# Kernel tuning notes

Measured on AMD Instinct MI355X. Metric: run time of the kernel, lower is better.

The kernel has to match this reference:

```python
import jax, jax.numpy as jnp
import numpy as np

B, N, D_IN, D_OUT = 4, 2048, 1024, 1024

def setup_inputs() -> dict:
    key = jax.random.key(0)
    ks = jax.random.split(key, 7)
    s_in = 1.0 / np.sqrt(D_IN)
    return {
        "X": jax.random.normal(ks[0], (B, N, D_IN), dtype=jnp.float32),
        "Wq": jax.random.uniform(ks[1], (D_IN, D_OUT), jnp.float32, -s_in, s_in),
        "bq": jax.random.uniform(ks[2], (D_OUT,), jnp.float32, -s_in, s_in),
        "Wk": jax.random.uniform(ks[3], (D_IN, D_OUT), jnp.float32, -s_in, s_in),
        "bk": jax.random.uniform(ks[4], (D_OUT,), jnp.float32, -s_in, s_in),
        "Wv": jax.random.uniform(ks[5], (D_IN, D_OUT), jnp.float32, -s_in, s_in),
        "bv": jax.random.uniform(ks[6], (D_OUT,), jnp.float32, -s_in, s_in),
    }

def reference(X, Wq, bq, Wk, bk, Wv, bv):
    # QKV projections: [B,N,D_in] @ [D_in,D_out] -> [B,N,D_out]
    q = jnp.einsum('bnd,de->bne', X, Wq) + bq
    k = jnp.einsum('bnd,de->bne', X, Wk) + bk
    v = jnp.einsum('bnd,de->bne', X, Wv) + bv
    # Unscaled attention (faithful: original has no 1/sqrt(d))
    scores = jnp.einsum('bne,bme->bnm', q, k)  # [B,N,N]
    weights = jax.nn.softmax(scores, axis=-1)
    return jnp.einsum('bnm,bme->bne', weights, v)
```

## Files before the change

### kernel.cpp

```cpp
#include <hip/hip_runtime.h>
#include <hip/hip_bf16.h>
#include <hip/hip_fp16.h>
#include <stdint.h>
#include <math.h>


typedef unsigned short ushort_t;
typedef __attribute__((ext_vector_type(8))) _Float16  f16x8;
typedef __attribute__((ext_vector_type(4))) _Float16  f16x4;
typedef __attribute__((ext_vector_type(4))) float     f32x4;

__device__ __forceinline__ void async_load16(const void* g, void* l) {
  __builtin_amdgcn_global_load_lds(
      (const __attribute__((address_space(1))) void*)g,
      (__attribute__((address_space(3))) void*)l, 16, 0, 0);
}

#define BARR do { __builtin_amdgcn_sched_barrier(0); \
                  __builtin_amdgcn_s_barrier();      \
                  __builtin_amdgcn_sched_barrier(0); } while (0)

#define A0OFF 0
#define B0OFF 16384
#define A1OFF 32768
#define B1OFF 49152

template<int SHIFT>
__device__ __forceinline__ void stage_half(const ushort_t* __restrict__ gb,
                                           int k0, int q, ushort_t* lt, int t)
{
#pragma unroll
  for (int j = 0; j < 2; ++j) {
    const int i   = j * 64 + (t >> 3);
    const int row = ((i >> SHIFT) << (SHIFT + 1)) | (q << SHIFT) | (i & ((1 << SHIFT) - 1));
    const int ch  = (t & 7) ^ (row & 7);
    async_load16(gb + (long)row * 1024 + k0 + ch * 8, lt + row * 64 + (t & 7) * 8);
  }
}

#define RD_A(TP, QM)                                                          \
  do { _Pragma("unroll") for (int m_ = 0; m_ < 4; ++m_) {                     \
    af[m_][0] = *(const f16x8*)&(TP)[(arow0 + (QM)*64 + m_*16) * 64 + ck0];   \
    af[m_][1] = *(const f16x8*)&(TP)[(arow0 + (QM)*64 + m_*16) * 64 + ck1];   \
  } } while (0)

#define RD_B(TP, QN)                                                          \
  do { _Pragma("unroll") for (int n_ = 0; n_ < 2; ++n_) {                     \
    bf[n_][0] = *(const f16x8*)&(TP)[(brow0 + (QN)*32 + n_*16) * 64 + ck0];   \
    bf[n_][1] = *(const f16x8*)&(TP)[(brow0 + (QN)*32 + n_*16) * 64 + ck1];   \
  } } while (0)

#define MM(QM, QN)                                                            \
  do { __builtin_amdgcn_s_setprio(1);                                         \
  _Pragma("unroll") for (int kh_ = 0; kh_ < 2; ++kh_)                         \
    _Pragma("unroll") for (int m_ = 0; m_ < 4; ++m_)                          \
      _Pragma("unroll") for (int n_ = 0; n_ < 2; ++n_)                        \
        acc[(QM)*4+m_][(QN)*2+n_] = __builtin_amdgcn_mfma_f32_16x16x32_f16(   \
            af[m_][kh_], bf[n_][kh_], acc[(QM)*4+m_][(QN)*2+n_], 0, 0, 0);    \
  __builtin_amdgcn_s_setprio(0); } while (0)

template<bool LAST>
__device__ __forceinline__ void iter256(const ushort_t* __restrict__ Ab,
                                        const ushort_t* __restrict__ Bb,
                                        ushort_t* lds, f32x4 (&acc)[8][4],
                                        int ka, int t, int arow0, int brow0,
                                        int ck0, int ck1)
{
  const int kb = ka + 64, kc = ka + 128, kd = ka + 192;
  f16x8 af[4][2], bf[2][2];

  RD_A(lds + A0OFF, 0); RD_B(lds + B0OFF, 0);
  stage_half<5>(Bb, kb, 0, lds + B1OFF, t);
  BARR; MM(0, 0); BARR;

  RD_B(lds + B0OFF, 1);
  if constexpr (!LAST) stage_half<6>(Ab, kc, 0, lds + A0OFF, t);
  BARR; MM(0, 1); BARR;

  RD_A(lds + A0OFF, 1);
  if constexpr (!LAST) stage_half<5>(Bb, kc, 1, lds + B0OFF, t);
  BARR; MM(1, 1); BARR;

  RD_B(lds + B0OFF, 0);
  if constexpr (!LAST) stage_half<6>(Ab, kc, 1, lds + A0OFF, t);
  BARR; MM(1, 0);
  if constexpr (LAST) asm volatile("s_waitcnt vmcnt(0)" ::: "memory");
  else                asm volatile("s_waitcnt vmcnt(6)" ::: "memory");
  BARR;

  RD_A(lds + A1OFF, 0); RD_B(lds + B1OFF, 0);
  if constexpr (!LAST) stage_half<5>(Bb, kc, 0, lds + B0OFF, t);
  BARR; MM(0, 0); BARR;

  RD_B(lds + B1OFF, 1);
  if constexpr (!LAST) stage_half<6>(Ab, kd, 0, lds + A1OFF, t);
  BARR; MM(0, 1); BARR;

  RD_A(lds + A1OFF, 1);
  if constexpr (!LAST) stage_half<5>(Bb, kd, 1, lds + B1OFF, t);
  BARR; MM(1, 1); BARR;

  RD_B(lds + B1OFF, 0);
  if constexpr (!LAST) stage_half<6>(Ab, kd, 1, lds + A1OFF, t);
  BARR; MM(1, 0);
  if constexpr (!LAST) asm volatile("s_waitcnt vmcnt(6)" ::: "memory");
  BARR;
}

__device__ __forceinline__ void gemm256(const ushort_t* __restrict__ Ab,
                                        const ushort_t* __restrict__ Bb,
                                        ushort_t* lds, f32x4 (&acc)[8][4])
{
  const int t    = threadIdx.x;
  const int lane = t & 63;
  const int wave = t >> 6;
  const int wr   = wave >> 2;
  const int wc   = wave & 3;
  const int arow0 = wr * 128 + (lane & 15);
  const int brow0 = wc * 64  + (lane & 15);
  const int ck0 = (((lane >> 4)    ) ^ (lane & 7)) * 8;
  const int ck1 = ((4 + (lane >> 4)) ^ (lane & 7)) * 8;

  stage_half<6>(Ab,  0, 0, lds + A0OFF, t);
  stage_half<5>(Bb,  0, 1, lds + B0OFF, t);
  stage_half<6>(Ab,  0, 1, lds + A0OFF, t);
  stage_half<5>(Bb,  0, 0, lds + B0OFF, t);
  stage_half<6>(Ab, 64, 0, lds + A1OFF, t);
  stage_half<5>(Bb, 64, 1, lds + B1OFF, t);
  stage_half<6>(Ab, 64, 1, lds + A1OFF, t);
  asm volatile("s_waitcnt vmcnt(6)" ::: "memory");
  BARR;

#pragma unroll 1
  for (int it = 0; it < 7; ++it)
    iter256<false>(Ab, Bb, lds, acc, it * 128, t, arow0, brow0, ck0, ck1);
  iter256<true>(Ab, Bb, lds, acc, 896, t, arow0, brow0, ck0, ck1);
}

#define NA0 0
#define NB0 16384
#define NA1 24576
#define NB1 40960

__device__ __forceinline__ void stage_A_n(const ushort_t* __restrict__ gb, long ldk,
                                          int k0, int q, ushort_t* lt, int t)
{
#pragma unroll
  for (int j = 0; j < 2; ++j) {
    const int i   = j * 64 + (t >> 3);
    const int row = ((i >> 5) << 6) | (q << 5) | (i & 31);
    const int ch  = (t & 7) ^ (row & 7);
    async_load16(gb + (long)row * ldk + k0 + ch * 8, lt + row * 64 + (t & 7) * 8);
  }
}

__device__ __forceinline__ void stage_B_n(const ushort_t* __restrict__ gb, long ldk,
                                          int k0, int q, ushort_t* lt, int t)
{
  const int i   = t >> 3;
  const int row = ((i >> 5) << 6) | (q << 5) | (i & 31);
  const int ch  = (t & 7) ^ (row & 7);
  async_load16(gb + (long)row * ldk + k0 + ch * 8, lt + row * 64 + (t & 7) * 8);
}

#define RDN_A(TP, QM)                                                         \
  do { _Pragma("unroll") for (int m_ = 0; m_ < 2; ++m_) {                     \
    af[m_][0] = *(const f16x8*)&(TP)[(arow_l + (QM)*32 + m_*16) * 64 + ck0];  \
    af[m_][1] = *(const f16x8*)&(TP)[(arow_l + (QM)*32 + m_*16) * 64 + ck1];  \
  } } while (0)

#define RDN_AS(TP, QM, S)                                                     \
  do { _Pragma("unroll") for (int m_ = 0; m_ < 2; ++m_) {                     \
    af[m_][0] = *(const f16x8*)&(TP)[(arow_l + (QM)*32 + m_*16) * 64 + ck0] * (S)[(QM)*2+m_]; \
    af[m_][1] = *(const f16x8*)&(TP)[(arow_l + (QM)*32 + m_*16) * 64 + ck1] * (S)[(QM)*2+m_]; \
  } } while (0)

#define RDN_B(TP, QN)                                                         \
  do { _Pragma("unroll") for (int n_ = 0; n_ < 2; ++n_) {                     \
    bf[n_][0] = *(const f16x8*)&(TP)[(brow_l + (QN)*32 + n_*16) * 64 + ck0];  \
    bf[n_][1] = *(const f16x8*)&(TP)[(brow_l + (QN)*32 + n_*16) * 64 + ck1];  \
  } } while (0)

#define MMN(QM, QN)                                                           \
  do { __builtin_amdgcn_s_setprio(1);                                         \
  _Pragma("unroll") for (int kh_ = 0; kh_ < 2; ++kh_)                         \
    _Pragma("unroll") for (int m_ = 0; m_ < 2; ++m_)                          \
      _Pragma("unroll") for (int n_ = 0; n_ < 2; ++n_)                        \
        acc[(QM)*2+m_][(QN)*2+n_] = __builtin_amdgcn_mfma_f32_16x16x32_f16(   \
            af[m_][kh_], bf[n_][kh_], acc[(QM)*2+m_][(QN)*2+n_], 0, 0, 0);    \
  __builtin_amdgcn_s_setprio(0); } while (0)

template<bool LAST>
__device__ __forceinline__ void iter_n(const ushort_t* __restrict__ Ab,
                                       const ushort_t* __restrict__ Bb,
                                       long lda, long ldb,
                                       ushort_t* lds, f32x4 (&acc)[4][4],
                                       int ka, int t, int arow_l, int brow_l,
                                       int ck0, int ck1)
{
  const int kb = ka + 64, kc = ka + 128, kd = ka + 192;
  f16x8 af[2][2], bf[2][2];

  RDN_A(lds + NA0, 0); RDN_B(lds + NB0, 0);
  stage_B_n(Bb, ldb, kb, 0, lds + NB1, t);
  BARR; MMN(0, 0); BARR;

  RDN_B(lds + NB0, 1);
  if constexpr (!LAST) stage_A_n(Ab, lda, kc, 0, lds + NA0, t);
  BARR; MMN(0, 1); BARR;

  RDN_A(lds + NA0, 1);
  if constexpr (!LAST) stage_B_n(Bb, ldb, kc, 1, lds + NB0, t);
  BARR; MMN(1, 1); BARR;

  RDN_B(lds + NB0, 0);
  if constexpr (!LAST) stage_A_n(Ab, lda, kc, 1, lds + NA0, t);
  BARR; MMN(1, 0);
  if constexpr (LAST) asm volatile("s_waitcnt vmcnt(0)" ::: "memory");
  else                asm volatile("s_waitcnt vmcnt(5)" ::: "memory");
  BARR;

  RDN_A(lds + NA1, 0); RDN_B(lds + NB1, 0);
  if constexpr (!LAST) stage_B_n(Bb, ldb, kc, 0, lds + NB0, t);
  BARR; MMN(0, 0); BARR;

  RDN_B(lds + NB1, 1);
  if constexpr (!LAST) stage_A_n(Ab, lda, kd, 0, lds + NA1, t);
  BARR; MMN(0, 1); BARR;

  RDN_A(lds + NA1, 1);
  if constexpr (!LAST) stage_B_n(Bb, ldb, kd, 1, lds + NB1, t);
  BARR; MMN(1, 1); BARR;

  RDN_B(lds + NB1, 0);
  if constexpr (!LAST) stage_A_n(Ab, lda, kd, 1, lds + NA1, t);
  BARR; MMN(1, 0);
  if constexpr (!LAST) asm volatile("s_waitcnt vmcnt(5)" ::: "memory");
  BARR;
}

template<bool LAST>
__device__ __forceinline__ void pv_iter_n(const ushort_t* __restrict__ Ab,
                                          const ushort_t* __restrict__ Bb,
                                          ushort_t* lds, f32x4 (&acc)[4][4],
                                          int ka, int t, int arow_l, int brow_l,
                                          int ck0, int ck1,
                                          float (&scc)[2][4],
                                          const float* __restrict__ Scb, int arow_abs)
{
  const int kb = ka + 64, kc = ka + 128, kd = ka + 192;
  f16x8 af[2][2], bf[2][2];

  float scn[2][4];
  if constexpr (!LAST) {
    const int cbn = (ka >> 6) + 2;
#pragma unroll
    for (int h = 0; h < 2; ++h)
#pragma unroll
      for (int s = 0; s < 4; ++s)
        scn[h][s] = Scb[(long)(cbn + h) * 2048 + arow_abs + s * 16];
  }
  _Float16 sa[4], sb[4];
#pragma unroll
  for (int s = 0; s < 4; ++s) { sa[s] = (_Float16)scc[0][s]; sb[s] = (_Float16)scc[1][s]; }

  RDN_AS(lds + NA0, 0, sa); RDN_B(lds + NB0, 0);
  stage_B_n(Bb, 2048, kb, 0, lds + NB1, t);
  BARR; MMN(0, 0); BARR;

  RDN_B(lds + NB0, 1);
  if constexpr (!LAST) stage_A_n(Ab, 2048, kc, 0, lds + NA0, t);
  BARR; MMN(0, 1); BARR;

  RDN_AS(lds + NA0, 1, sa);
  if constexpr (!LAST) stage_B_n(Bb, 2048, kc, 1, lds + NB0, t);
  BARR; MMN(1, 1); BARR;

  RDN_B(lds + NB0, 0);
  if constexpr (!LAST) stage_A_n(Ab, 2048, kc, 1, lds + NA0, t);
  BARR; MMN(1, 0);
  if constexpr (LAST) asm volatile("s_waitcnt vmcnt(0)" ::: "memory");
  else                asm volatile("s_waitcnt vmcnt(5)" ::: "memory");
  BARR;

  RDN_AS(lds + NA1, 0, sb); RDN_B(lds + NB1, 0);
  if constexpr (!LAST) stage_B_n(Bb, 2048, kc, 0, lds + NB0, t);
  BARR; MMN(0, 0); BARR;

  RDN_B(lds + NB1, 1);
  if constexpr (!LAST) stage_A_n(Ab, 2048, kd, 0, lds + NA1, t);
  BARR; MMN(0, 1); BARR;

  RDN_AS(lds + NA1, 1, sb);
  if constexpr (!LAST) stage_B_n(Bb, 2048, kd, 1, lds + NB1, t);
  BARR; MMN(1, 1); BARR;

  RDN_B(lds + NB1, 0);
  if constexpr (!LAST) stage_A_n(Ab, 2048, kd, 1, lds + NA1, t);
  BARR; MMN(1, 0);
  if constexpr (!LAST) asm volatile("s_waitcnt vmcnt(5)" ::: "memory");
  BARR;

  if constexpr (!LAST) {
#pragma unroll
    for (int h = 0; h < 2; ++h)
#pragma unroll
      for (int s = 0; s < 4; ++s) scc[h][s] = scn[h][s];
  }
}

#define PROLOGUE_N(LDA, LDB)                                \
  do {                                                      \
    stage_A_n(Ab, (LDA),  0, 0, lds + NA0, t);              \
    stage_B_n(Bb, (LDB),  0, 0, lds + NB0, t);              \
    stage_A_n(Ab, (LDA),  0, 1, lds + NA0, t);              \
    stage_B_n(Bb, (LDB),  0, 1, lds + NB0, t);              \
    stage_A_n(Ab, (LDA), 64, 0, lds + NA1, t);              \
    stage_B_n(Bb, (LDB), 64, 1, lds + NB1, t);              \
    stage_A_n(Ab, (LDA), 64, 1, lds + NA1, t);              \
    asm volatile("s_waitcnt vmcnt(5)" ::: "memory");        \
    BARR;                                                   \
  } while (0)

__global__ __launch_bounds__(512, 2)
void qkv128n_kernel(const ushort_t* __restrict__ A, const ushort_t* __restrict__ BT,
                    const float* __restrict__ bq, const float* __restrict__ bk,
                    const float* __restrict__ bvp,
                    __half* __restrict__ Qh, __half* __restrict__ Kh,
                    ushort_t* __restrict__ Vt)
{
  __shared__ __align__(16) ushort_t lds[49152];

  const int nb = gridDim.x * gridDim.y;
  int id = blockIdx.y * gridDim.x + blockIdx.x;
  id = (id & 7) * (nb >> 3) + (id >> 3);
  const int bx = id % gridDim.x;
  const int by = id / gridDim.x;

  const ushort_t* Ab = A  + (long)by * 256 * 1024;
  const ushort_t* Bb = BT + (long)bx * 128 * 1024;

  const int t    = threadIdx.x;
  const int lane = t & 63;
  const int wave = t >> 6;
  const int wr   = wave >> 1;
  const int wc   = wave & 1;
  const int arow_l = wr * 64 + (lane & 15);
  const int brow_l = wc * 64 + (lane & 15);
  const int ck0 = (((lane >> 4)    ) ^ (lane & 7)) * 8;
  const int ck1 = ((4 + (lane >> 4)) ^ (lane & 7)) * 8;

  f32x4 acc[4][4];
  const f32x4 zero = {0.0f, 0.0f, 0.0f, 0.0f};
#pragma unroll
  for (int i = 0; i < 4; ++i)
#pragma unroll
    for (int j = 0; j < 4; ++j) acc[i][j] = zero;

  PROLOGUE_N(1024, 1024);
#pragma unroll 1
  for (int it = 0; it < 7; ++it)
    iter_n<false>(Ab, Bb, 1024, 1024, lds, acc, it * 128, t, arow_l, brow_l, ck0, ck1);
  iter_n<true>(Ab, Bb, 1024, 1024, lds, acc, 896, t, arow_l, brow_l, ck0, ck1);

  const int er = (lane >> 4) * 4, ec = lane & 15;
  const int tgt = bx >> 3;
  const float* bias = (tgt == 0) ? bq : (tgt == 1) ? bk : bvp;

#pragma unroll
  for (int ni = 0; ni < 4; ++ni) {
    const int col = (bx & 7) * 128 + wc * 64 + ni * 16 + ec;
    const float bval = bias[col];
#pragma unroll
    for (int mi = 0; mi < 4; ++mi) {
      const long grow0 = (long)by * 256 + wr * 64 + mi * 16 + er;
      if (tgt < 2) {
        __half* o = (tgt == 0) ? Qh : Kh;
#pragma unroll
        for (int r = 0; r < 4; ++r)
          o[(grow0 + r) * 1024 + col] = __float2half(acc[mi][ni][r] + bval);
      } else {
        const long b  = grow0 >> 11;
        const long ml = grow0 & 2047;
        f16x4 v4;
#pragma unroll
        for (int r = 0; r < 4; ++r) v4[r] = (_Float16)(acc[mi][ni][r] + bval);
        *(f16x4*)&Vt[b * 2097152 + (long)col * 2048 + ml] = v4;
      }
    }
  }
}

__global__ __launch_bounds__(512, 2)
void qk256_kernel(const ushort_t* __restrict__ Q, const ushort_t* __restrict__ Kh,
                  __half* __restrict__ S, float* __restrict__ PM, float* __restrict__ PS)
{
  __shared__ __align__(16) ushort_t lds[65536];

  const int nb = gridDim.x * gridDim.y;
  int id = blockIdx.y * gridDim.x + blockIdx.x;
  id = (id & 7) * (nb >> 3) + (id >> 3);
  const int bx = id % gridDim.x;
  const int by = id / gridDim.x;
  const long z = blockIdx.z;

  const ushort_t* Ab = Q  + z * 2048 * 1024 + (long)by * 256 * 1024;
  const ushort_t* Bb = Kh + z * 2048 * 1024 + (long)bx * 256 * 1024;
  __half* Sb = S + z * 2048 * 2048;

  f32x4 acc[8][4];
  const f32x4 zero = {0.0f, 0.0f, 0.0f, 0.0f};
#pragma unroll
  for (int i = 0; i < 8; ++i)
#pragma unroll
    for (int j = 0; j < 4; ++j) acc[i][j] = zero;

  gemm256(Ab, Bb, lds, acc);

  const int t = threadIdx.x, lane = t & 63, wave = t >> 6;
  const int wr = wave >> 2, wc = wave & 3;
  const int er = (lane >> 4) * 4, ec = lane & 15;
  const int cc = bx * 4 + wc;
  float* PMb = PM + z * 32 * 2048 + (long)cc * 2048;
  float* PSb = PS + z * 32 * 2048 + (long)cc * 2048;

#pragma unroll
  for (int m8 = 0; m8 < 8; ++m8)
#pragma unroll
    for (int r = 0; r < 4; ++r) {
      float m = fmaxf(fmaxf(acc[m8][0][r], acc[m8][1][r]),
                      fmaxf(acc[m8][2][r], acc[m8][3][r]));
      m = fmaxf(m, __shfl_xor(m, 1));
      m = fmaxf(m, __shfl_xor(m, 2));
      m = fmaxf(m, __shfl_xor(m, 4));
      m = fmaxf(m, __shfl_xor(m, 8));
      float s = 0.0f;
#pragma unroll
      for (int n4 = 0; n4 < 4; ++n4) {
        const float e = __expf(acc[m8][n4][r] - m);
        acc[m8][n4][r] = e;
        s += e;
      }
      s += __shfl_xor(s, 1);
      s += __shfl_xor(s, 2);
      s += __shfl_xor(s, 4);
      s += __shfl_xor(s, 8);
      if (ec == 0) {
        const long row = (long)by * 256 + wr * 128 + m8 * 16 + er + r;
        PMb[row] = m;
        PSb[row] = s;
      }
    }

#pragma unroll
  for (int n4 = 0; n4 < 4; ++n4) {
    const long col = (long)bx * 256 + wc * 64 + n4 * 16 + ec;
#pragma unroll
    for (int m8 = 0; m8 < 8; ++m8)
#pragma unroll
      for (int r = 0; r < 4; ++r) {
        const long grow = (long)by * 256 + wr * 128 + m8 * 16 + er + r;
        Sb[grow * 2048 + col] = __float2half(acc[m8][n4][r]);
      }
  }
}

__global__ __launch_bounds__(256)
void softmax_reduce_kernel(const float* __restrict__ PM, const float* __restrict__ PS,
                           float* __restrict__ Sc)
{
  const int r = blockIdx.x * 256 + threadIdx.x;
  const int b = r >> 11, row = r & 2047;
  const long base = (long)b * 32 * 2048 + row;
  float m = -3.4e38f;
#pragma unroll
  for (int cb = 0; cb < 32; ++cb) m = fmaxf(m, PM[base + cb * 2048]);
  float l = 0.0f;
#pragma unroll
  for (int cb = 0; cb < 32; ++cb) l += PS[base + cb * 2048] * __expf(PM[base + cb * 2048] - m);
  const float inv = 1.0f / l;
#pragma unroll
  for (int cb = 0; cb < 32; ++cb) Sc[base + cb * 2048] = __expf(PM[base + cb * 2048] - m) * inv;
}

__global__ __launch_bounds__(512, 2)
void pv128n_kernel(const ushort_t* __restrict__ S, const ushort_t* __restrict__ Vt,
                   const float* __restrict__ Sc, float* __restrict__ Out)
{
  __shared__ __align__(16) ushort_t lds[49152];

  const int nb = gridDim.x * gridDim.y;
  int id = blockIdx.y * gridDim.x + blockIdx.x;
  id = (id & 7) * (nb >> 3) + (id >> 3);
  const int bx = id % gridDim.x;
  const int by = id / gridDim.x;
  const long z = blockIdx.z;

  const ushort_t* Ab = S  + z * 4194304 + (long)by * 256 * 2048;
  const ushort_t* Bb = Vt + z * 2097152 + (long)bx * 128 * 2048;
  const float* Scb = Sc + z * 32 * 2048;
  float* Cb = Out + z * 2048 * 1024;

  const int t    = threadIdx.x;
  const int lane = t & 63;
  const int wave = t >> 6;
  const int wr   = wave >> 1;
  const int wc   = wave & 1;
  const int arow_l = wr * 64 + (lane & 15);
  const int brow_l = wc * 64 + (lane & 15);
  const int arow_abs = by * 256 + arow_l;
  const int ck0 = (((lane >> 4)    ) ^ (lane & 7)) * 8;
  const int ck1 = ((4 + (lane >> 4)) ^ (lane & 7)) * 8;

  f32x4 acc[4][4];
  const f32x4 zero = {0.0f, 0.0f, 0.0f, 0.0f};
#pragma unroll
  for (int i = 0; i < 4; ++i)
#pragma unroll
    for (int j = 0; j < 4; ++j) acc[i][j] = zero;

  float scc[2][4];
#pragma unroll
  for (int h = 0; h < 2; ++h)
#pragma unroll
    for (int s = 0; s < 4; ++s)
      scc[h][s] = Scb[(long)h * 2048 + arow_abs + s * 16];

  PROLOGUE_N(2048, 2048);
#pragma unroll 1
  for (int it = 0; it < 15; ++it)
    pv_iter_n<false>(Ab, Bb, lds, acc, it * 128, t, arow_l, brow_l, ck0, ck1,
                     scc, Scb, arow_abs);
  pv_iter_n<true>(Ab, Bb, lds, acc, 1920, t, arow_l, brow_l, ck0, ck1,
                  scc, Scb, arow_abs);

  const int er = (lane >> 4) * 4, ec = lane & 15;
#pragma unroll
  for (int ni = 0; ni < 4; ++ni) {
    const int gcol = bx * 128 + wc * 64 + ni * 16 + ec;
#pragma unroll
    for (int mi = 0; mi < 4; ++mi) {
#pragma unroll
      for (int r = 0; r < 4; ++r) {
        const long grow = (long)by * 256 + wr * 64 + mi * 16 + er + r;
        Cb[grow * 1024 + gcol] = acc[mi][ni][r];
      }
    }
  }
}

__global__ __launch_bounds__(256)
void cvt_f32_f16_kernel(const float* __restrict__ src, __half* __restrict__ dst, long n)
{
  const long i = ((long)blockIdx.x * 256 + threadIdx.x) * 8;
  if (i + 8 > n) return;
  const float4 a = *(const float4*)(src + i);
  const float4 b = *(const float4*)(src + i + 4);
  f16x8 h;
  h[0] = (_Float16)a.x; h[1] = (_Float16)a.y; h[2] = (_Float16)a.z; h[3] = (_Float16)a.w;
  h[4] = (_Float16)b.x; h[5] = (_Float16)b.y; h[6] = (_Float16)b.z; h[7] = (_Float16)b.w;
  *(f16x8*)((ushort_t*)dst + i) = h;
}

__global__ __launch_bounds__(256)
void transpose_cvt3_kernel(const float* __restrict__ W0, const float* __restrict__ W1,
                           const float* __restrict__ W2, __half* __restrict__ dst)
{
  __shared__ float tile[32][33];
  const int z = blockIdx.z;
  const float* src = (z == 0) ? W0 : (z == 1) ? W1 : W2;
  __half* d = dst + (long)z * 1024 * 1024;
  const int c0 = blockIdx.x * 32;
  const int r0 = blockIdx.y * 32;
  const int tx = threadIdx.x & 31;
  const int ty = threadIdx.x >> 5;
#pragma unroll
  for (int i = 0; i < 32; i += 8)
    tile[ty + i][tx] = src[(long)(r0 + ty + i) * 1024 + (c0 + tx)];
  __syncthreads();
#pragma unroll
  for (int i = 0; i < 32; i += 8)
    d[(long)(c0 + ty + i) * 1024 + (r0 + tx)] = __float2half(tile[tx][ty + i]);
}

extern "C" void kernel_launch(void* const* d_in, const int* in_sizes, int n_in,
                              void* d_out, int out_size, void* d_ws, size_t ws_size,
                              hipStream_t stream)
{
  const int  Bb = 4, Nn = 2048, Dd = 1024;
  const long BN = (long)Bb * Nn;

  const float* X  = (const float*)d_in[0];
  const float* Wq = (const float*)d_in[1];
  const float* bq = (const float*)d_in[2];
  const float* Wk = (const float*)d_in[3];
  const float* bk = (const float*)d_in[4];
  const float* Wv = (const float*)d_in[5];
  const float* bv = (const float*)d_in[6];
  float* Out      = (float*)d_out;

  uint8_t* w = (uint8_t*)d_ws;
  ushort_t* Wt = (ushort_t*)w;  w += (size_t)3 * Dd * Dd * 2;

  transpose_cvt3_kernel<<<dim3(Dd / 32, Dd / 32, 3), 256, 0, stream>>>(Wq, Wk, Wv, (__half*)Wt);

  const size_t statsBytes = (size_t)Bb * 32 * Nn * 4;
  const size_t fullNeed = (size_t)3 * Dd * Dd * 2
                        + 4 * ((size_t)BN * Dd * 2)
                        + (size_t)Bb * Nn * Nn * 2
                        + 3 * statsBytes;

  if (ws_size >= fullNeed) {
    ushort_t* Xh = (ushort_t*)w;  w += (size_t)BN * Dd * 2;
    ushort_t* Q  = (ushort_t*)w;  w += (size_t)BN * Dd * 2;
    ushort_t* Kb = (ushort_t*)w;  w += (size_t)BN * Dd * 2;
    ushort_t* Vt = (ushort_t*)w;  w += (size_t)BN * Dd * 2;
    ushort_t* S  = (ushort_t*)w;  w += (size_t)Bb * Nn * Nn * 2;
    float*    PM = (float*)w;     w += statsBytes;
    float*    PS = (float*)w;     w += statsBytes;
    float*    Sc = (float*)w;

    cvt_f32_f16_kernel<<<dim3((unsigned)(BN * Dd / (8 * 256))), 256, 0, stream>>>(
        X, (__half*)Xh, BN * Dd);

    qkv128n_kernel<<<dim3(3 * Dd / 128, BN / 256, 1), 512, 0, stream>>>(
        Xh, Wt, bq, bk, bv, (__half*)Q, (__half*)Kb, Vt);

    qk256_kernel<<<dim3(Nn / 256, Nn / 256, Bb), 512, 0, stream>>>(
        Q, Kb, (__half*)S, PM, PS);

    softmax_reduce_kernel<<<dim3((unsigned)(Bb * Nn / 256)), 256, 0, stream>>>(PM, PS, Sc);

    pv128n_kernel<<<dim3(Dd / 128, Nn / 256, Bb), 512, 0, stream>>>(
        S, Vt, Sc, Out);
  } else {
    ushort_t* Xh = (ushort_t*)w;  w += (size_t)Nn * Dd * 2;
    ushort_t* Q  = (ushort_t*)w;  w += (size_t)Nn * Dd * 2;
    ushort_t* Kb = (ushort_t*)w;  w += (size_t)Nn * Dd * 2;
    ushort_t* Vt = (ushort_t*)w;  w += (size_t)Nn * Dd * 2;
    ushort_t* S  = (ushort_t*)w;  w += (size_t)Nn * Nn * 2;
    float*    PM = (float*)w;     w += (size_t)32 * Nn * 4;
    float*    PS = (float*)w;     w += (size_t)32 * Nn * 4;
    float*    Sc = (float*)w;

    for (int b = 0; b < Bb; ++b) {
      const float* Xb = X + (long)b * Nn * Dd;
      cvt_f32_f16_kernel<<<dim3((unsigned)((long)Nn * Dd / (8 * 256))), 256, 0, stream>>>(
          Xb, (__half*)Xh, (long)Nn * Dd);
      qkv128n_kernel<<<dim3(3 * Dd / 128, Nn / 256, 1), 512, 0, stream>>>(
          Xh, Wt, bq, bk, bv, (__half*)Q, (__half*)Kb, Vt);
      qk256_kernel<<<dim3(Nn / 256, Nn / 256, 1), 512, 0, stream>>>(
          Q, Kb, (__half*)S, PM, PS);
      softmax_reduce_kernel<<<dim3((unsigned)(Nn / 256)), 256, 0, stream>>>(PM, PS, Sc);
      pv128n_kernel<<<dim3(Dd / 128, Nn / 256, 1), 512, 0, stream>>>(
          S, Vt, Sc, Out + (long)b * Nn * Dd);
    }
  }
}
```

Measured before the change: 267.3 us.

## Fuse softmax reduce into PV, merge prep kernels, restructure GEMM inner pipeline

The softmax row-statistics reduction is folded into the PV kernel: each block computes per-chunk scale factors into shared memory rather than reading a separate Sc buffer. The weight transpose and X conversion are merged into one prep launch. The GEMM inner loop now reads both B column-halves at once and runs 4 MFMA phases per 128-K step instead of 8, which halves the barriers and changes the staging order and vmcnt thresholds. This removes two launches and a global round trip for the scales. In exchange each PV block recomputes the row reduction, adds 32KB of shared memory, and holds more registers.

```diff
diff --git a/kernel.cpp b/kernel.cpp
--- a/kernel.cpp
+++ b/kernel.cpp
@@ -175,159 +175,143 @@
     af[m_][1] = *(const f16x8*)&(TP)[(arow_l + (QM)*32 + m_*16) * 64 + ck1] * (S)[(QM)*2+m_]; \
   } } while (0)
 
-#define RDN_B(TP, QN)                                                         \
+#define RDN_B2(TP, QN, BF)                                                    \
   do { _Pragma("unroll") for (int n_ = 0; n_ < 2; ++n_) {                     \
-    bf[n_][0] = *(const f16x8*)&(TP)[(brow_l + (QN)*32 + n_*16) * 64 + ck0];  \
-    bf[n_][1] = *(const f16x8*)&(TP)[(brow_l + (QN)*32 + n_*16) * 64 + ck1];  \
+    (BF)[n_][0] = *(const f16x8*)&(TP)[(brow_l + (QN)*32 + n_*16) * 64 + ck0];\
+    (BF)[n_][1] = *(const f16x8*)&(TP)[(brow_l + (QN)*32 + n_*16) * 64 + ck1];\
   } } while (0)
 
-#define MMN(QM, QN)                                                           \
+#define MM2(QM)                                                               \
   do { __builtin_amdgcn_s_setprio(1);                                         \
   _Pragma("unroll") for (int kh_ = 0; kh_ < 2; ++kh_)                         \
     _Pragma("unroll") for (int m_ = 0; m_ < 2; ++m_)                          \
-      _Pragma("unroll") for (int n_ = 0; n_ < 2; ++n_)                        \
-        acc[(QM)*2+m_][(QN)*2+n_] = __builtin_amdgcn_mfma_f32_16x16x32_f16(   \
-            af[m_][kh_], bf[n_][kh_], acc[(QM)*2+m_][(QN)*2+n_], 0, 0, 0);    \
+      _Pragma("unroll") for (int n_ = 0; n_ < 2; ++n_) {                      \
+        acc[(QM)*2+m_][n_]   = __builtin_amdgcn_mfma_f32_16x16x32_f16(        \
+            af[m_][kh_], bq0[n_][kh_], acc[(QM)*2+m_][n_], 0, 0, 0);          \
+        acc[(QM)*2+m_][2+n_] = __builtin_amdgcn_mfma_f32_16x16x32_f16(        \
+            af[m_][kh_], bq1[n_][kh_], acc[(QM)*2+m_][2+n_], 0, 0, 0);        \
+      }                                                                       \
   __builtin_amdgcn_s_setprio(0); } while (0)
 
 template<bool LAST>
-__device__ __forceinline__ void iter_n(const ushort_t* __restrict__ Ab,
-                                       const ushort_t* __restrict__ Bb,
-                                       long lda, long ldb,
-                                       ushort_t* lds, f32x4 (&acc)[4][4],
-                                       int ka, int t, int arow_l, int brow_l,
-                                       int ck0, int ck1)
+__device__ __forceinline__ void iter4_n(const ushort_t* __restrict__ Ab,
+                                        const ushort_t* __restrict__ Bb,
+                                        long lda, long ldb,
+                                        ushort_t* lds, f32x4 (&acc)[4][4],
+                                        int ka, int t, int arow_l, int brow_l,
+                                        int ck0, int ck1)
 {
   const int kb = ka + 64, kc = ka + 128, kd = ka + 192;
-  f16x8 af[2][2], bf[2][2];
-
-  RDN_A(lds + NA0, 0); RDN_B(lds + NB0, 0);
-  stage_B_n(Bb, ldb, kb, 0, lds + NB1, t);
-  BARR; MMN(0, 0); BARR;
-
-  RDN_B(lds + NB0, 1);
-  if constexpr (!LAST) stage_A_n(Ab, lda, kc, 0, lds + NA0, t);
-  BARR; MMN(0, 1); BARR;
+  f16x8 af[2][2], bq0[2][2], bq1[2][2];
+
+  RDN_A(lds + NA0, 0);
+  RDN_B2(lds + NB0, 0, bq0);
+  RDN_B2(lds + NB0, 1, bq1);
+  stage_B_n(Bb, ldb, kb, 1, lds + NB1, t);
+  stage_A_n(Ab, lda, kb, 1, lds + NA1, t);
+  BARR; MM2(0); BARR;
 
   RDN_A(lds + NA0, 1);
-  if constexpr (!LAST) stage_B_n(Bb, ldb, kc, 1, lds + NB0, t);
-  BARR; MMN(1, 1); BARR;
-
-  RDN_B(lds + NB0, 0);
-  if constexpr (!LAST) stage_A_n(Ab, lda, kc, 1, lds + NA0, t);
-  BARR; MMN(1, 0);
+  if constexpr (!LAST) {
+    stage_A_n(Ab, lda, kc, 0, lds + NA0, t);
+    stage_B_n(Bb, ldb, kc, 0, lds + NB0, t);
+  }
+  BARR; MM2(1);
   if constexpr (LAST) asm volatile("s_waitcnt vmcnt(0)" ::: "memory");
-  else                asm volatile("s_waitcnt vmcnt(5)" ::: "memory");
+  else                asm volatile("s_waitcnt vmcnt(3)" ::: "memory");
   BARR;
 
-  RDN_A(lds + NA1, 0); RDN_B(lds + NB1, 0);
-  if constexpr (!LAST) stage_B_n(Bb, ldb, kc, 0, lds + NB0, t);
-  BARR; MMN(0, 0); BARR;
-
-  RDN_B(lds + NB1, 1);
-  if constexpr (!LAST) stage_A_n(Ab, lda, kd, 0, lds + NA1, t);
-  BARR; MMN(0, 1); BARR;
+  RDN_A(lds + NA1, 0);
+  RDN_B2(lds + NB1, 0, bq0);
+  RDN_B2(lds + NB1, 1, bq1);
+  if constexpr (!LAST) {
+    stage_B_n(Bb, ldb, kc, 1, lds + NB0, t);
+    stage_A_n(Ab, lda, kc, 1, lds + NA0, t);
+  }
+  BARR; MM2(0); BARR;
 
   RDN_A(lds + NA1, 1);
-  if constexpr (!LAST) stage_B_n(Bb, ldb, kd, 1, lds + NB1, t);
-  BARR; MMN(1, 1); BARR;
-
-  RDN_B(lds + NB1, 0);
-  if constexpr (!LAST) stage_A_n(Ab, lda, kd, 1, lds + NA1, t);
-  BARR; MMN(1, 0);
-  if constexpr (!LAST) asm volatile("s_waitcnt vmcnt(5)" ::: "memory");
+  if constexpr (!LAST) {
+    stage_A_n(Ab, lda, kd, 0, lds + NA1, t);
+    stage_B_n(Bb, ldb, kd, 0, lds + NB1, t);
+  }
+  BARR; MM2(1);
+  if constexpr (!LAST) asm volatile("s_waitcnt vmcnt(3)" ::: "memory");
   BARR;
 }
 
 template<bool LAST>
-__device__ __forceinline__ void pv_iter_n(const ushort_t* __restrict__ Ab,
-                                          const ushort_t* __restrict__ Bb,
-                                          ushort_t* lds, f32x4 (&acc)[4][4],
-                                          int ka, int t, int arow_l, int brow_l,
-                                          int ck0, int ck1,
-                                          float (&scc)[2][4],
-                                          const float* __restrict__ Scb, int arow_abs)
+__device__ __forceinline__ void pv_iter4(const ushort_t* __restrict__ Ab,
+                                         const ushort_t* __restrict__ Bb,
+                                         ushort_t* lds, const float (*ScL)[256],
+                                         f32x4 (&acc)[4][4],
+                                         int ka, int t, int arow_l, int brow_l,
+                                         int ck0, int ck1)
 {
   const int kb = ka + 64, kc = ka + 128, kd = ka + 192;
-  f16x8 af[2][2], bf[2][2];
-
-  float scn[2][4];
+  const int cba = ka >> 6;
+  f16x8 af[2][2], bq0[2][2], bq1[2][2];
+  _Float16 sa[4], sb[4];
+#pragma unroll
+  for (int s = 0; s < 4; ++s) {
+    sa[s] = (_Float16)ScL[cba][arow_l + s * 16];
+    sb[s] = (_Float16)ScL[cba + 1][arow_l + s * 16];
+  }
+
+  RDN_AS(lds + NA0, 0, sa);
+  RDN_B2(lds + NB0, 0, bq0);
+  RDN_B2(lds + NB0, 1, bq1);
+  stage_B_n(Bb, 2048, kb, 1, lds + NB1, t);
+  stage_A_n(Ab, 2048, kb, 1, lds + NA1, t);
+  BARR; MM2(0); BARR;
+
+  RDN_AS(lds + NA0, 1, sa);
   if constexpr (!LAST) {
-    const int cbn = (ka >> 6) + 2;
-#pragma unroll
-    for (int h = 0; h < 2; ++h)
-#pragma unroll
-      for (int s = 0; s < 4; ++s)
-        scn[h][s] = Scb[(long)(cbn + h) * 2048 + arow_abs + s * 16];
-  }
-  _Float16 sa[4], sb[4];
-#pragma unroll
-  for (int s = 0; s < 4; ++s) { sa[s] = (_Float16)scc[0][s]; sb[s] = (_Float16)scc[1][s]; }
-
-  RDN_AS(lds + NA0, 0, sa); RDN_B(lds + NB0, 0);
-  stage_B_n(Bb, 2048, kb, 0, lds + NB1, t);
-  BARR; MMN(0, 0); BARR;
-
-  RDN_B(lds + NB0, 1);
-  if constexpr (!LAST) stage_A_n(Ab, 2048, kc, 0, lds + NA0, t);
-  BARR; MMN(0, 1); BARR;
-
-  RDN_AS(lds + NA0, 1, sa);
-  if constexpr (!LAST) stage_B_n(Bb, 2048, kc, 1, lds + NB0, t);
-  BARR; MMN(1, 1); BARR;
-
-  RDN_B(lds + NB0, 0);
-  if constexpr (!LAST) stage_A_n(Ab, 2048, kc, 1, lds + NA0, t);
-  BARR; MMN(1, 0);
+    stage_A_n(Ab, 2048, kc, 0, lds + NA0, t);
+    stage_B_n(Bb, 2048, kc, 0, lds + NB0, t);
+  }
+  BARR; MM2(1);
   if constexpr (LAST) asm volatile("s_waitcnt vmcnt(0)" ::: "memory");
-  else                asm volatile("s_waitcnt vmcnt(5)" ::: "memory");
+  else                asm volatile("s_waitcnt vmcnt(3)" ::: "memory");
   BARR;
 
-  RDN_AS(lds + NA1, 0, sb); RDN_B(lds + NB1, 0);
-  if constexpr (!LAST) stage_B_n(Bb, 2048, kc, 0, lds + NB0, t);
-  BARR; MMN(0, 0); BARR;
-
-  RDN_B(lds + NB1, 1);
-  if constexpr (!LAST) stage_A_n(Ab, 2048, kd, 0, lds + NA1, t);
-  BARR; MMN(0, 1); BARR;
+  RDN_AS(lds + NA1, 0, sb);
+  RDN_B2(lds + NB1, 0, bq0);
+  RDN_B2(lds + NB1, 1, bq1);
+  if constexpr (!LAST) {
+    stage_B_n(Bb, 2048, kc, 1, lds + NB0, t);
+    stage_A_n(Ab, 2048, kc, 1, lds + NA0, t);
+  }
+  BARR; MM2(0); BARR;
 
   RDN_AS(lds + NA1, 1, sb);
-  if constexpr (!LAST) stage_B_n(Bb, 2048, kd, 1, lds + NB1, t);
-  BARR; MMN(1, 1); BARR;
-
-  RDN_B(lds + NB1, 0);
-  if constexpr (!LAST) stage_A_n(Ab, 2048, kd, 1, lds + NA1, t);
-  BARR; MMN(1, 0);
-  if constexpr (!LAST) asm volatile("s_waitcnt vmcnt(5)" ::: "memory");
+  if constexpr (!LAST) {
+    stage_A_n(Ab, 2048, kd, 0, lds + NA1, t);
+    stage_B_n(Bb, 2048, kd, 0, lds + NB1, t);
+  }
+  BARR; MM2(1);
+  if constexpr (!LAST) asm volatile("s_waitcnt vmcnt(3)" ::: "memory");
   BARR;
-
-  if constexpr (!LAST) {
-#pragma unroll
-    for (int h = 0; h < 2; ++h)
-#pragma unroll
-      for (int s = 0; s < 4; ++s) scc[h][s] = scn[h][s];
-  }
-}
-
-#define PROLOGUE_N(LDA, LDB)                                \
+}
+
+#define PROLOGUE4(LDA, LDB)                                 \
   do {                                                      \
     stage_A_n(Ab, (LDA),  0, 0, lds + NA0, t);              \
     stage_B_n(Bb, (LDB),  0, 0, lds + NB0, t);              \
+    stage_B_n(Bb, (LDB),  0, 1, lds + NB0, t);              \
     stage_A_n(Ab, (LDA),  0, 1, lds + NA0, t);              \
-    stage_B_n(Bb, (LDB),  0, 1, lds + NB0, t);              \
     stage_A_n(Ab, (LDA), 64, 0, lds + NA1, t);              \
-    stage_B_n(Bb, (LDB), 64, 1, lds + NB1, t);              \
-    stage_A_n(Ab, (LDA), 64, 1, lds + NA1, t);              \
-    asm volatile("s_waitcnt vmcnt(5)" ::: "memory");        \
+    stage_B_n(Bb, (LDB), 64, 0, lds + NB1, t);              \
+    asm volatile("s_waitcnt vmcnt(3)" ::: "memory");        \
     BARR;                                                   \
   } while (0)
 
 __global__ __launch_bounds__(512, 2)
-void qkv128n_kernel(const ushort_t* __restrict__ A, const ushort_t* __restrict__ BT,
-                    const float* __restrict__ bq, const float* __restrict__ bk,
-                    const float* __restrict__ bvp,
-                    __half* __restrict__ Qh, __half* __restrict__ Kh,
-                    ushort_t* __restrict__ Vt)
+void qkv4_kernel(const ushort_t* __restrict__ A, const ushort_t* __restrict__ BT,
+                 const float* __restrict__ bq, const float* __restrict__ bk,
+                 const float* __restrict__ bvp,
+                 __half* __restrict__ Qh, __half* __restrict__ Kh,
+                 ushort_t* __restrict__ Vt)
 {
   __shared__ __align__(16) ushort_t lds[49152];
 
@@ -357,11 +341,11 @@
 #pragma unroll
     for (int j = 0; j < 4; ++j) acc[i][j] = zero;
 
-  PROLOGUE_N(1024, 1024);
+  PROLOGUE4(1024, 1024);
 #pragma unroll 1
   for (int it = 0; it < 7; ++it)
-    iter_n<false>(Ab, Bb, 1024, 1024, lds, acc, it * 128, t, arow_l, brow_l, ck0, ck1);
-  iter_n<true>(Ab, Bb, 1024, 1024, lds, acc, 896, t, arow_l, brow_l, ck0, ck1);
+    iter4_n<false>(Ab, Bb, 1024, 1024, lds, acc, it * 128, t, arow_l, brow_l, ck0, ck1);
+  iter4_n<true>(Ab, Bb, 1024, 1024, lds, acc, 896, t, arow_l, brow_l, ck0, ck1);
 
   const int er = (lane >> 4) * 4, ec = lane & 15;
   const int tgt = bx >> 3;
@@ -465,29 +449,13 @@
   }
 }
 
-__global__ __launch_bounds__(256)
-void softmax_reduce_kernel(const float* __restrict__ PM, const float* __restrict__ PS,
-                           float* __restrict__ Sc)
-{
-  const int r = blockIdx.x * 256 + threadIdx.x;
-  const int b = r >> 11, row = r & 2047;
-  const long base = (long)b * 32 * 2048 + row;
-  float m = -3.4e38f;
-#pragma unroll
-  for (int cb = 0; cb < 32; ++cb) m = fmaxf(m, PM[base + cb * 2048]);
-  float l = 0.0f;
-#pragma unroll
-  for (int cb = 0; cb < 32; ++cb) l += PS[base + cb * 2048] * __expf(PM[base + cb * 2048] - m);
-  const float inv = 1.0f / l;
-#pragma unroll
-  for (int cb = 0; cb < 32; ++cb) Sc[base + cb * 2048] = __expf(PM[base + cb * 2048] - m) * inv;
-}
-
 __global__ __launch_bounds__(512, 2)
-void pv128n_kernel(const ushort_t* __restrict__ S, const ushort_t* __restrict__ Vt,
-                   const float* __restrict__ Sc, float* __restrict__ Out)
+void pv4_kernel(const ushort_t* __restrict__ S, const ushort_t* __restrict__ Vt,
+                const float* __restrict__ PM, const float* __restrict__ PS,
+                float* __restrict__ Out)
 {
   __shared__ __align__(16) ushort_t lds[49152];
+  __shared__ float ScL[32][256];
 
   const int nb = gridDim.x * gridDim.y;
   int id = blockIdx.y * gridDim.x + blockIdx.x;
@@ -498,17 +466,38 @@
 
   const ushort_t* Ab = S  + z * 4194304 + (long)by * 256 * 2048;
   const ushort_t* Bb = Vt + z * 2097152 + (long)bx * 128 * 2048;
-  const float* Scb = Sc + z * 32 * 2048;
   float* Cb = Out + z * 2048 * 1024;
 
-  const int t    = threadIdx.x;
+  const int t = threadIdx.x;
+
+  if (t < 256) {
+    const long row = (long)by * 256 + t;
+    const float* PMb = PM + z * 32 * 2048;
+    const float* PSb = PS + z * 32 * 2048;
+    float pm[32];
+    float m = -3.4e38f;
+#pragma unroll
+    for (int cb = 0; cb < 32; ++cb) {
+      pm[cb] = PMb[(long)cb * 2048 + row];
+      m = fmaxf(m, pm[cb]);
+    }
+    float l = 0.0f;
+#pragma unroll
+    for (int cb = 0; cb < 32; ++cb)
+      l += PSb[(long)cb * 2048 + row] * __expf(pm[cb] - m);
+    const float inv = 1.0f / l;
+#pragma unroll
+    for (int cb = 0; cb < 32; ++cb)
+      ScL[cb][t] = __expf(pm[cb] - m) * inv;
+  }
+  __syncthreads();
+
   const int lane = t & 63;
   const int wave = t >> 6;
   const int wr   = wave >> 1;
   const int wc   = wave & 1;
   const int arow_l = wr * 64 + (lane & 15);
   const int brow_l = wc * 64 + (lane & 15);
-  const int arow_abs = by * 256 + arow_l;
   const int ck0 = (((lane >> 4)    ) ^ (lane & 7)) * 8;
   const int ck1 = ((4 + (lane >> 4)) ^ (lane & 7)) * 8;
 
@@ -519,20 +508,11 @@
 #pragma unroll
     for (int j = 0; j < 4; ++j) acc[i][j] = zero;
 
-  float scc[2][4];
-#pragma unroll
-  for (int h = 0; h < 2; ++h)
-#pragma unroll
-    for (int s = 0; s < 4; ++s)
-      scc[h][s] = Scb[(long)h * 2048 + arow_abs + s * 16];
-
-  PROLOGUE_N(2048, 2048);
+  PROLOGUE4(2048, 2048);
 #pragma unroll 1
   for (int it = 0; it < 15; ++it)
-    pv_iter_n<false>(Ab, Bb, lds, acc, it * 128, t, arow_l, brow_l, ck0, ck1,
-                     scc, Scb, arow_abs);
-  pv_iter_n<true>(Ab, Bb, lds, acc, 1920, t, arow_l, brow_l, ck0, ck1,
-                  scc, Scb, arow_abs);
+    pv_iter4<false>(Ab, Bb, lds, ScL, acc, it * 128, t, arow_l, brow_l, ck0, ck1);
+  pv_iter4<true>(Ab, Bb, lds, ScL, acc, 1920, t, arow_l, brow_l, ck0, ck1);
 
   const int er = (lane >> 4) * 4, ec = lane & 15;
 #pragma unroll
@@ -546,6 +526,39 @@
         Cb[grow * 1024 + gcol] = acc[mi][ni][r];
       }
     }
+  }
+}
+
+__global__ __launch_bounds__(256)
+void prep_kernel(const float* __restrict__ W0, const float* __restrict__ W1,
+                 const float* __restrict__ W2, __half* __restrict__ dstW,
+                 const float* __restrict__ X, __half* __restrict__ Xh)
+{
+  __shared__ float tile[32][33];
+  const int z = blockIdx.z;
+  if (z < 3) {
+    const float* src = (z == 0) ? W0 : (z == 1) ? W1 : W2;
+    __half* d = dstW + (long)z * 1024 * 1024;
+    const int c0 = blockIdx.x * 32;
+    const int r0 = blockIdx.y * 32;
+    const int tx = threadIdx.x & 31;
+    const int ty = threadIdx.x >> 5;
+#pragma unroll
+    for (int i = 0; i < 32; i += 8)
+      tile[ty + i][tx] = src[(long)(r0 + ty + i) * 1024 + (c0 + tx)];
+    __syncthreads();
+#pragma unroll
+    for (int i = 0; i < 32; i += 8)
+      d[(long)(c0 + ty + i) * 1024 + (r0 + tx)] = __float2half(tile[tx][ty + i]);
+  } else {
+    const int bid = blockIdx.y * gridDim.x + blockIdx.x;
+    const long i = (((long)(z - 3) * 1024 + bid) * 256 + threadIdx.x) * 8;
+    const float4 a = *(const float4*)(X + i);
+    const float4 b = *(const float4*)(X + i + 4);
+    f16x8 h;
+    h[0] = (_Float16)a.x; h[1] = (_Float16)a.y; h[2] = (_Float16)a.z; h[3] = (_Float16)a.w;
+    h[4] = (_Float16)b.x; h[5] = (_Float16)b.y; h[6] = (_Float16)b.z; h[7] = (_Float16)b.w;
+    *(f16x8*)((ushort_t*)Xh + i) = h;
   }
 }
 
@@ -602,13 +615,11 @@
   uint8_t* w = (uint8_t*)d_ws;
   ushort_t* Wt = (ushort_t*)w;  w += (size_t)3 * Dd * Dd * 2;
 
-  transpose_cvt3_kernel<<<dim3(Dd / 32, Dd / 32, 3), 256, 0, stream>>>(Wq, Wk, Wv, (__half*)Wt);
-
   const size_t statsBytes = (size_t)Bb * 32 * Nn * 4;
   const size_t fullNeed = (size_t)3 * Dd * Dd * 2
                         + 4 * ((size_t)BN * Dd * 2)
                         + (size_t)Bb * Nn * Nn * 2
-                        + 3 * statsBytes;
+                        + 2 * statsBytes;
 
   if (ws_size >= fullNeed) {
     ushort_t* Xh = (ushort_t*)w;  w += (size_t)BN * Dd * 2;
@@ -617,22 +628,18 @@
     ushort_t* Vt = (ushort_t*)w;  w += (size_t)BN * Dd * 2;
     ushort_t* S  = (ushort_t*)w;  w += (size_t)Bb * Nn * Nn * 2;
     float*    PM = (float*)w;     w += statsBytes;
-    float*    PS = (float*)w;     w += statsBytes;
-    float*    Sc = (float*)w;
-
-    cvt_f32_f16_kernel<<<dim3((unsigned)(BN * Dd / (8 * 256))), 256, 0, stream>>>(
-        X, (__half*)Xh, BN * Dd);
-
-    qkv128n_kernel<<<dim3(3 * Dd / 128, BN / 256, 1), 512, 0, stream>>>(
+    float*    PS = (float*)w;
+
+    prep_kernel<<<dim3(32, 32, 7), 256, 0, stream>>>(Wq, Wk, Wv, (__half*)Wt, X, (__half*)Xh);
+
+    qkv4_kernel<<<dim3(3 * Dd / 128, BN / 256, 1), 512, 0, stream>>>(
         Xh, Wt, bq, bk, bv, (__half*)Q, (__half*)Kb, Vt);
 
     qk256_kernel<<<dim3(Nn / 256, Nn / 256, Bb), 512, 0, stream>>>(
         Q, Kb, (__half*)S, PM, PS);
 
-    softmax_reduce_kernel<<<dim3((unsigned)(Bb * Nn / 256)), 256, 0, stream>>>(PM, PS, Sc);
-
-    pv128n_kernel<<<dim3(Dd / 128, Nn / 256, Bb), 512, 0, stream>>>(
-        S, Vt, Sc, Out);
+    pv4_kernel<<<dim3(Dd / 128, Nn / 256, Bb), 512, 0, stream>>>(
+        S, Vt, PM, PS, Out);
   } else {
     ushort_t* Xh = (ushort_t*)w;  w += (size_t)Nn * Dd * 2;
     ushort_t* Q  = (ushort_t*)w;  w += (size_t)Nn * Dd * 2;
@@ -640,20 +647,20 @@
     ushort_t* Vt = (ushort_t*)w;  w += (size_t)Nn * Dd * 2;
     ushort_t* S  = (ushort_t*)w;  w += (size_t)Nn * Nn * 2;
     float*    PM = (float*)w;     w += (size_t)32 * Nn * 4;
-    float*    PS = (float*)w;     w += (size_t)32 * Nn * 4;
-    float*    Sc = (float*)w;
+    float*    PS = (float*)w;
+
+    transpose_cvt3_kernel<<<dim3(Dd / 32, Dd / 32, 3), 256, 0, stream>>>(Wq, Wk, Wv, (__half*)Wt);
 
     for (int b = 0; b < Bb; ++b) {
       const float* Xb = X + (long)b * Nn * Dd;
       cvt_f32_f16_kernel<<<dim3((unsigned)((long)Nn * Dd / (8 * 256))), 256, 0, stream>>>(
           Xb, (__half*)Xh, (long)Nn * Dd);
-      qkv128n_kernel<<<dim3(3 * Dd / 128, Nn / 256, 1), 512, 0, stream>>>(
+      qkv4_kernel<<<dim3(3 * Dd / 128, Nn / 256, 1), 512, 0, stream>>>(
           Xh, Wt, bq, bk, bv, (__half*)Q, (__half*)Kb, Vt);
       qk256_kernel<<<dim3(Nn / 256, Nn / 256, 1), 512, 0, stream>>>(
           Q, Kb, (__half*)S, PM, PS);
-      softmax_reduce_kernel<<<dim3((unsigned)(Nn / 256)), 256, 0, stream>>>(PM, PS, Sc);
-      pv128n_kernel<<<dim3(Dd / 128, Nn / 256, 1), 512, 0, stream>>>(
-          S, Vt, Sc, Out + (long)b * Nn * Dd);
+      pv4_kernel<<<dim3(Dd / 128, Nn / 256, 1), 512, 0, stream>>>(
+          S, Vt, PM, PS, Out + (long)b * Nn * Dd);
     }
   }
 }
```

Result: faster. 261.1 us (-2.3%).
